# Kernel optimization log

Measured on AMD Instinct MI355X. Metric: run time of the kernel, lower is better.

Reference implementation:

```python
import jax, jax.numpy as jnp
import numpy as np

N_NODES = 20000
N_EDGES = 320000
D_IN = 128
D_OUT = 128
HEADS = 12
BN_EPS = 1e-5


def setup_inputs() -> dict:
    key = jax.random.key(0)
    ks = jax.random.split(key, 24)
    x = jax.random.normal(ks[0], (N_NODES, D_IN), dtype=jnp.float32)
    # edges guaranteed to have no self loops (so remove_self_loops is a no-op)
    src = jax.random.randint(ks[1], (N_EDGES,), 0, N_NODES, dtype=jnp.int32)
    off = jax.random.randint(ks[2], (N_EDGES,), 1, N_NODES, dtype=jnp.int32)
    dst = (src + off) % N_NODES
    edge_index = jnp.stack([src, dst], axis=0)
    inp = {"x": x, "edge_index": edge_index}
    # per-layer FeatureSteeredConvolution params (torch init: uniform weights, N(0,0.1) c/bias)
    dims_in = [D_IN, D_OUT, D_OUT]
    k = 3
    for li in range(3):
        din = dims_in[li]
        inp[f"l{li}_Wlin"] = jax.random.uniform(ks[k], (HEADS * D_OUT, din), dtype=jnp.float32); k += 1
        inp[f"l{li}_Wu"] = jax.random.uniform(ks[k], (HEADS, din), dtype=jnp.float32); k += 1
        inp[f"l{li}_c"] = 0.1 * jax.random.normal(ks[k], (HEADS,), dtype=jnp.float32); k += 1
        inp[f"l{li}_b"] = 0.1 * jax.random.normal(ks[k], (D_OUT,), dtype=jnp.float32); k += 1
    for bi in range(2):
        inp[f"bn{bi}_g"] = jnp.ones((D_OUT,), dtype=jnp.float32)
        inp[f"bn{bi}_b"] = jnp.zeros((D_OUT,), dtype=jnp.float32)
    return inp


def _fsc(x, src, dst, Wlin, Wu, c, b):
    """FeatureSteeredConvolution: edge gather -> softmax attention over heads ->
    per-head linear -> scatter-mean over destination nodes."""
    n = x.shape[0]
    x_j = x[src]                                  # [E, Cin] source features
    x_i = x[dst]                                  # [E, Cin] target features
    att = jax.nn.softmax((x_i - x_j) @ Wu.T + c, axis=1)   # [E, H]
    Wl = Wlin.reshape(HEADS, D_OUT, -1)           # [H, Cout, Cin]
    msg = jnp.zeros((src.shape[0], D_OUT), dtype=x.dtype)
    for h in range(HEADS):                        # small fixed loop over heads
        msg = msg + att[:, h:h + 1] * (x_j @ Wl[h].T)
    agg = jax.ops.segment_sum(msg, dst, num_segments=n)
    deg = jax.ops.segment_sum(jnp.ones((dst.shape[0],), dtype=x.dtype), dst, num_segments=n)
    return agg / jnp.maximum(deg, 1.0)[:, None] + b


def _bn(x, g, b):
    # BatchNorm1d in training mode: biased batch statistics
    m = jnp.mean(x, axis=0)
    v = jnp.var(x, axis=0)
    return (x - m) * jax.lax.rsqrt(v + BN_EPS) * g + b


def reference(x, edge_index, l0_Wlin, l0_Wu, l0_c, l0_b, bn0_g, bn0_b,
              l1_Wlin, l1_Wu, l1_c, l1_b, bn1_g, bn1_b,
              l2_Wlin, l2_Wu, l2_c, l2_b):
    n = x.shape[0]
    loops = jnp.arange(n, dtype=edge_index.dtype)
    src = jnp.concatenate([edge_index[0], loops])
    dst = jnp.concatenate([edge_index[1], loops])
    h = jax.nn.relu(_fsc(x, src, dst, l0_Wlin, l0_Wu, l0_c, l0_b))
    h = _bn(h, bn0_g, bn0_b)
    h = jax.nn.relu(_fsc(h, src, dst, l1_Wlin, l1_Wu, l1_c, l1_b))
    h = _bn(h, bn1_g, bn1_b)
    return _fsc(h, src, dst, l2_Wlin, l2_Wu, l2_c, l2_b)
```

## Files before the change

kernel.cpp:

```cpp
#include <hip/hip_runtime.h>
#include <hip/hip_bf16.h>

#define DHID 128
#define NH 12
#define KDIM 1536
#define KSPLIT 3
#define KS (KDIM / KSPLIT)
#define NSTATB 128

typedef __attribute__((ext_vector_type(8))) short short8;
typedef __attribute__((ext_vector_type(4))) float f32x4;

static __device__ __forceinline__ unsigned short f2bf(float f) {
  __hip_bfloat16 h = __float2bfloat16(f);
  return __builtin_bit_cast(unsigned short, h);
}


__global__ void hist_k(const int* __restrict__ dstp, int* __restrict__ cnt, int e0, int et) {
  int e = blockIdx.x * blockDim.x + threadIdx.x;
  if (e >= et) return;
  int d = (e < e0) ? dstp[e] : (e - e0);
  atomicAdd(&cnt[d], 1);
}

__global__ void scan_k(const int* __restrict__ cnt, int* __restrict__ row_start,
                       int* __restrict__ cursor, int n, int total) {
  __shared__ int part[1024];
  int t = threadIdx.x;
  const int CH = (n + 1023) >> 10;
  int base = t * CH;
  int s = 0;
  for (int j = 0; j < CH; ++j) { int i = base + j; if (i < n) s += cnt[i]; }
  part[t] = s;
  __syncthreads();
  for (int off = 1; off < 1024; off <<= 1) {
    int v = (t >= off) ? part[t - off] : 0;
    __syncthreads();
    part[t] += v;
    __syncthreads();
  }
  int run = (t == 0) ? 0 : part[t - 1];
  for (int j = 0; j < CH; ++j) {
    int i = base + j;
    if (i < n) {
      int c = cnt[i];
      row_start[i] = run;
      cursor[i] = run;
      run += c;
    }
  }
  if (t == 0) row_start[n] = total;
}

__global__ void scatter_k(const int* __restrict__ srcp, const int* __restrict__ dstp,
                          int* __restrict__ cursor, int* __restrict__ srcs,
                          int* __restrict__ dsts, int e0, int et) {
  int e = blockIdx.x * blockDim.x + threadIdx.x;
  if (e >= et) return;
  int s = (e < e0) ? srcp[e] : (e - e0);
  int d = (e < e0) ? dstp[e] : (e - e0);
  int pos = atomicAdd(&cursor[d], 1);
  srcs[pos] = s;
  dsts[pos] = d;
}


__global__ void u_k(const float* __restrict__ x, const float* __restrict__ Wu,
                    float* __restrict__ u, int n) {
  int wid = (blockIdx.x * blockDim.x + threadIdx.x) >> 6;
  if (wid >= n) return;
  int lane = threadIdx.x & 63;
  float2 xv = *(const float2*)(x + (long)wid * DHID + 2 * lane);
  #pragma unroll
  for (int h = 0; h < NH; ++h) {
    float2 wv = *(const float2*)(Wu + h * DHID + 2 * lane);
    float p = xv.x * wv.x + xv.y * wv.y;
    p += __shfl_xor(p, 1);  p += __shfl_xor(p, 2);  p += __shfl_xor(p, 4);
    p += __shfl_xor(p, 8);  p += __shfl_xor(p, 16); p += __shfl_xor(p, 32);
    if (lane == 0) u[wid * NH + h] = p;
  }
}


__global__ void att_k(const float* __restrict__ u, const float* __restrict__ cvec,
                      const int* __restrict__ srcs, const int* __restrict__ dsts,
                      const int* __restrict__ row_start, float* __restrict__ attS, int et) {
  int j = blockIdx.x * blockDim.x + threadIdx.x;
  if (j >= et) return;
  int s = srcs[j], d = dsts[j];
  const float4* ud = (const float4*)(u + (long)d * NH);
  const float4* us = (const float4*)(u + (long)s * NH);
  const float4* cp = (const float4*)cvec;
  float w[NH];
  #pragma unroll
  for (int q = 0; q < 3; ++q) {
    float4 a = ud[q], b = us[q], c = cp[q];
    w[4*q+0] = a.x - b.x + c.x;
    w[4*q+1] = a.y - b.y + c.y;
    w[4*q+2] = a.z - b.z + c.z;
    w[4*q+3] = a.w - b.w + c.w;
  }
  float m = w[0];
  #pragma unroll
  for (int h = 1; h < NH; ++h) m = fmaxf(m, w[h]);
  float ssum = 0.f;
  #pragma unroll
  for (int h = 0; h < NH; ++h) { w[h] = __expf(w[h] - m); ssum += w[h]; }
  float deg = (float)(row_start[d + 1] - row_start[d]);
  float inv = 1.f / (ssum * deg);
  float4* op = (float4*)(attS + (long)j * NH);
  #pragma unroll
  for (int q = 0; q < 3; ++q) {
    float4 v;
    v.x = w[4*q+0] * inv; v.y = w[4*q+1] * inv;
    v.z = w[4*q+2] * inv; v.w = w[4*q+3] * inv;
    op[q] = v;
  }
}


__global__ void edge_k(const float* __restrict__ x, const float* __restrict__ attS,
                       const int* __restrict__ srcs, const int* __restrict__ row_start,
                       unsigned short* __restrict__ A, int n) {
  int wid = __builtin_amdgcn_readfirstlane((int)((blockIdx.x * blockDim.x + threadIdx.x) >> 6));
  if (wid >= n) return;
  int lane = threadIdx.x & 63;
  float acc[NH][2];
  #pragma unroll
  for (int h = 0; h < NH; ++h) { acc[h][0] = 0.f; acc[h][1] = 0.f; }
  int beg = row_start[wid], end = row_start[wid + 1];
  int j = beg;
  for (; j + 3 < end; j += 4) {
    int sx[4];
    #pragma unroll
    for (int i = 0; i < 4; ++i) sx[i] = srcs[j + i];
    float2 xv[4];
    #pragma unroll
    for (int i = 0; i < 4; ++i)
      xv[i] = *(const float2*)(x + (long)sx[i] * DHID + 2 * lane);
    const float4* ap = (const float4*)(attS + (long)j * NH);
    float4 aq[4][3];
    #pragma unroll
    for (int i = 0; i < 4; ++i) {
      aq[i][0] = ap[i * 3 + 0];
      aq[i][1] = ap[i * 3 + 1];
      aq[i][2] = ap[i * 3 + 2];
    }
    #pragma unroll
    for (int i = 0; i < 4; ++i) {
      float av[NH];
      av[0]=aq[i][0].x; av[1]=aq[i][0].y; av[2] =aq[i][0].z; av[3] =aq[i][0].w;
      av[4]=aq[i][1].x; av[5]=aq[i][1].y; av[6] =aq[i][1].z; av[7] =aq[i][1].w;
      av[8]=aq[i][2].x; av[9]=aq[i][2].y; av[10]=aq[i][2].z; av[11]=aq[i][2].w;
      #pragma unroll
      for (int h = 0; h < NH; ++h) {
        acc[h][0] += av[h] * xv[i].x;
        acc[h][1] += av[h] * xv[i].y;
      }
    }
  }
  for (; j < end; ++j) {
    int s0 = srcs[j];
    float2 xv0 = *(const float2*)(x + (long)s0 * DHID + 2 * lane);
    const float4* a0p = (const float4*)(attS + (long)j * NH);
    float4 a00 = a0p[0], a01 = a0p[1], a02 = a0p[2];
    float av0[NH];
    av0[0]=a00.x; av0[1]=a00.y; av0[2]=a00.z;  av0[3]=a00.w;
    av0[4]=a01.x; av0[5]=a01.y; av0[6]=a01.z;  av0[7]=a01.w;
    av0[8]=a02.x; av0[9]=a02.y; av0[10]=a02.z; av0[11]=a02.w;
    #pragma unroll
    for (int h = 0; h < NH; ++h) {
      acc[h][0] += av0[h] * xv0.x;
      acc[h][1] += av0[h] * xv0.y;
    }
  }
  unsigned* Ap = (unsigned*)(A + (long)wid * KDIM);
  #pragma unroll
  for (int h = 0; h < NH; ++h) {
    unsigned pv = (unsigned)f2bf(acc[h][0]) | ((unsigned)f2bf(acc[h][1]) << 16);
    Ap[h * (DHID / 2) + lane] = pv;
  }
}


__global__ void prep_wcat_k(const float* __restrict__ Wlin, unsigned short* __restrict__ Wcat) {
  int t = blockIdx.x * blockDim.x + threadIdx.x;
  int c = t / KDIM, f = t - c * KDIM;
  int h = f >> 7, k = f & (DHID - 1);
  Wcat[t] = f2bf(Wlin[((h << 7) + c) * DHID + k]);
}


__global__ __launch_bounds__(256) void gemm_k(
    const unsigned short* __restrict__ A, const unsigned short* __restrict__ B,
    float* __restrict__ part, float* __restrict__ outp, int M) {
  int w = threadIdx.x >> 6, lane = threadIdx.x & 63;
  int lr = lane & 15, lq = lane >> 4;
  int m0 = blockIdx.x * 64, n0 = w * 32;
  int ks = blockIdx.y;
  if (m0 >= M) return;
  f32x4 acc[4][2];
  #pragma unroll
  for (int mf = 0; mf < 4; ++mf)
    #pragma unroll
    for (int nf = 0; nf < 2; ++nf) acc[mf][nf] = (f32x4){0.f, 0.f, 0.f, 0.f};
  const short* Ap = (const short*)A;
  const short* Bp = (const short*)B;
  long arow[4], brow[2];
  #pragma unroll
  for (int mf = 0; mf < 4; ++mf) arow[mf] = (long)(m0 + mf * 16 + lr) * KDIM + lq * 8;
  #pragma unroll
  for (int nf = 0; nf < 2; ++nf) brow[nf] = (long)(n0 + nf * 16 + lr) * KDIM + lq * 8;
  const int kbeg = ks * KS, kend = kbeg + KS;
  #pragma unroll 2
  for (int kk = kbeg; kk < kend; kk += 32) {
    short8 av[4], bv[2];
    #pragma unroll
    for (int mf = 0; mf < 4; ++mf) av[mf] = *(const short8*)(Ap + arow[mf] + kk);
    #pragma unroll
    for (int nf = 0; nf < 2; ++nf) bv[nf] = *(const short8*)(Bp + brow[nf] + kk);
    #pragma unroll
    for (int mf = 0; mf < 4; ++mf)
      #pragma unroll
      for (int nf = 0; nf < 2; ++nf)
        acc[mf][nf] = __builtin_amdgcn_mfma_f32_16x16x32_bf16(av[mf], bv[nf], acc[mf][nf], 0, 0, 0);
  }
  float* op = (ks == 0) ? outp : (part + (long)(ks - 1) * M * DHID);
  #pragma unroll
  for (int mf = 0; mf < 4; ++mf) {
    #pragma unroll
    for (int nf = 0; nf < 2; ++nf) {
      int c = n0 + nf * 16 + lr;
      int rowb = m0 + mf * 16 + lq * 4;
      #pragma unroll
      for (int r = 0; r < 4; ++r) {
        int row = rowb + r;
        if (row < M) op[(long)row * DHID + c] = acc[mf][nf][r];
      }
    }
  }
}


__global__ void combine_k(const float* __restrict__ part, const float* __restrict__ bias,
                          float* __restrict__ outp, int M, int relu) {
  int t = blockIdx.x * blockDim.x + threadIdx.x;
  int nvec = M * (DHID / 4);
  if (t >= nvec) return;
  long idx = (long)t * 4;
  int c = (t & 31) * 4;
  float4 p0 = *(const float4*)(outp + idx);
  float4 p1 = *(const float4*)(part + idx);
  float4 p2 = *(const float4*)(part + (long)M * DHID + idx);
  float4 bc = *(const float4*)(bias + c);
  float4 v;
  v.x = p0.x + p1.x + p2.x + bc.x;
  v.y = p0.y + p1.y + p2.y + bc.y;
  v.z = p0.z + p1.z + p2.z + bc.z;
  v.w = p0.w + p1.w + p2.w + bc.w;
  if (relu) {
    v.x = fmaxf(v.x, 0.f); v.y = fmaxf(v.y, 0.f);
    v.z = fmaxf(v.z, 0.f); v.w = fmaxf(v.w, 0.f);
  }
  *(float4*)(outp + idx) = v;
}


__global__ __launch_bounds__(256) void bnstat_k(const float* __restrict__ buf,
                                                float* __restrict__ bnpart, int nvec) {
  int t = blockIdx.x * 256 + threadIdx.x;
  const int stride = NSTATB * 256;
  float s0=0,s1=0,s2=0,s3=0,q0=0,q1=0,q2=0,q3=0;
  for (int i = t; i < nvec; i += stride) {
    float4 v = *(const float4*)(buf + (long)i * 4);
    s0 += v.x; s1 += v.y; s2 += v.z; s3 += v.w;
    q0 += v.x*v.x; q1 += v.y*v.y; q2 += v.z*v.z; q3 += v.w*v.w;
  }
  s0 += __shfl_xor(s0, 32); s1 += __shfl_xor(s1, 32);
  s2 += __shfl_xor(s2, 32); s3 += __shfl_xor(s3, 32);
  q0 += __shfl_xor(q0, 32); q1 += __shfl_xor(q1, 32);
  q2 += __shfl_xor(q2, 32); q3 += __shfl_xor(q3, 32);
  __shared__ float red[4][256];
  int w = threadIdx.x >> 6, lane = threadIdx.x & 63;
  if (lane < 32) {
    int cb = lane * 4;
    red[w][cb+0] = s0; red[w][cb+1] = s1; red[w][cb+2] = s2; red[w][cb+3] = s3;
    red[w][128+cb+0] = q0; red[w][128+cb+1] = q1; red[w][128+cb+2] = q2; red[w][128+cb+3] = q3;
  }
  __syncthreads();
  int tt = threadIdx.x;
  float p = red[0][tt] + red[1][tt] + red[2][tt] + red[3][tt];
  bnpart[blockIdx.x * 256 + tt] = p;
}


__global__ void bnfin_k(const float* __restrict__ bnpart,
                        const float* __restrict__ g, const float* __restrict__ b,
                        float* __restrict__ sc, float* __restrict__ sh, float invn) {
  __shared__ float col[256];
  int t = threadIdx.x;
  float s = 0.f;
  #pragma unroll 8
  for (int bb = 0; bb < NSTATB; ++bb) s += bnpart[bb * 256 + t];
  col[t] = s;
  __syncthreads();
  if (t < DHID) {
    float m = col[t] * invn;
    float v = col[128 + t] * invn - m * m;
    float rs = rsqrtf(v + 1e-5f);
    float sg = g[t] * rs;
    sc[t] = sg;
    sh[t] = b[t] - m * sg;
  }
}

__global__ void bnapply_k(float* __restrict__ buf, const float* __restrict__ sc,
                          const float* __restrict__ sh, int nvec) {
  int i = blockIdx.x * blockDim.x + threadIdx.x;
  if (i >= nvec) return;
  long idx = (long)i * 4;
  int c = (int)(idx & (DHID - 1));
  float4 v = *(const float4*)(buf + idx);
  v.x = v.x * sc[c]     + sh[c];
  v.y = v.y * sc[c + 1] + sh[c + 1];
  v.z = v.z * sc[c + 2] + sh[c + 2];
  v.w = v.w * sc[c + 3] + sh[c + 3];
  *(float4*)(buf + idx) = v;
}


extern "C" void kernel_launch(void* const* d_in, const int* in_sizes, int n_in,
                              void* d_out, int out_size, void* d_ws, size_t ws_size,
                              hipStream_t stream) {
  const float* x = (const float*)d_in[0];
  const int* ei = (const int*)d_in[1];
  const int N = in_sizes[0] / DHID;
  const int E0 = in_sizes[1] / 2;
  const int ET = E0 + N;
  const int* srcp = ei;
  const int* dstp = ei + E0;
  const float* Wlin[3] = {(const float*)d_in[2], (const float*)d_in[6], (const float*)d_in[10]};
  const float* Wu[3]   = {(const float*)d_in[3], (const float*)d_in[7], (const float*)d_in[11]};
  const float* cc[3]   = {(const float*)d_in[4], (const float*)d_in[8], (const float*)d_in[12]};
  const float* bb[3]   = {(const float*)d_in[5], (const float*)d_in[9], (const float*)d_in[13]};
  const float* bng[2]  = {(const float*)d_in[14], (const float*)d_in[16]};
  const float* bnb[2]  = {(const float*)d_in[15], (const float*)d_in[17]};

  const int MPAD = ((N + 63) / 64) * 64;

  size_t o = 0;
  char* base = (char*)d_ws;
  auto carve = [&](size_t bytes) -> char* {
    char* p = base + o;
    o += (bytes + 255) & ~(size_t)255;
    return p;
  };
  int* row_start = (int*)carve((size_t)(N + 1) * 4);
  int* cursor    = (int*)carve((size_t)N * 4);
  int* srcs      = (int*)carve((size_t)ET * 4);
  int* dsts      = (int*)carve((size_t)ET * 4);
  float* u       = (float*)carve((size_t)N * NH * 4);
  float* bnpart  = (float*)carve((size_t)NSTATB * 256 * 4);
  float* bnsc    = (float*)carve((size_t)DHID * 4);
  float* bnsh    = (float*)carve((size_t)DHID * 4);
  unsigned short* Wcat = (unsigned short*)carve((size_t)DHID * KDIM * 2);
  size_t attS_bytes = (size_t)ET * NH * 4;
  size_t part_bytes = (size_t)(KSPLIT - 1) * N * DHID * 4;
  char* shared_rg = carve(attS_bytes > part_bytes ? attS_bytes : part_bytes);
  float* attS = (float*)shared_rg;
  float* partb = (float*)shared_rg;
  float* hA      = (float*)carve((size_t)N * DHID * 4);
  unsigned short* A = (unsigned short*)carve((size_t)MPAD * KDIM * 2);
  (void)ws_size; (void)n_in; (void)out_size;

  const int EB = (ET + 255) / 256;
  const int NW = (N + 3) / 4;
  const int MB64 = (N + 63) / 64;
  const int AV = (N * DHID / 4 + 255) / 256;

  hipMemsetAsync(cursor, 0, (size_t)N * 4, stream);
  hist_k<<<EB, 256, 0, stream>>>(dstp, cursor, E0, ET);
  scan_k<<<1, 1024, 0, stream>>>(cursor, row_start, cursor, N, ET);
  scatter_k<<<EB, 256, 0, stream>>>(srcp, dstp, cursor, srcs, dsts, E0, ET);

  const float* hin = x;
  for (int li = 0; li < 3; ++li) {
    const bool last = (li == 2);
    u_k<<<NW, 256, 0, stream>>>(hin, Wu[li], u, N);
    att_k<<<EB, 256, 0, stream>>>(u, cc[li], srcs, dsts, row_start, attS, ET);
    edge_k<<<NW, 256, 0, stream>>>(hin, attS, srcs, row_start, A, N);
    prep_wcat_k<<<(DHID * KDIM) / 256, 256, 0, stream>>>(Wlin[li], Wcat);
    float* outp = last ? (float*)d_out : hA;
    gemm_k<<<dim3(MB64, KSPLIT), 256, 0, stream>>>(A, Wcat, partb, outp, N);
    combine_k<<<AV, 256, 0, stream>>>(partb, bb[li], outp, N, last ? 0 : 1);
    if (!last) {
      bnstat_k<<<NSTATB, 256, 0, stream>>>(hA, bnpart, N * DHID / 4);
      bnfin_k<<<1, 256, 0, stream>>>(bnpart, bng[li], bnb[li], bnsc, bnsh, 1.f / (float)N);
      bnapply_k<<<AV, 256, 0, stream>>>(hA, bnsc, bnsh, N * DHID / 4);
      hin = hA;
    }
  }
}
```

Baseline: 543.1 us.

## Fuse BN stats into combine, fold BN apply into bf16 feature cast, prefetch GEMM

Batch-norm statistics are now accumulated inside the split-K combine kernel, and the BN scale/shift is applied inside u_k. u_k also writes a bf16 copy of the node features, so the separate bnstat and bnapply passes over the hidden buffer are removed. edge_k gathers the bf16 features instead of fp32, halving the gather bytes per edge. The GEMM inner loop now software-prefetches the next K slice into registers. The gathered features lose precision to bf16 before aggregation, and the combine runs as a fixed-size grid-stride kernel.

```diff
diff --git a/kernel.cpp b/kernel.cpp
--- a/kernel.cpp
+++ b/kernel.cpp
@@ -5,8 +5,8 @@
 #define NH 12
 #define KDIM 1536
 #define KSPLIT 3
-#define KS (KDIM / KSPLIT)
-#define NSTATB 128
+#define KSL (KDIM / KSPLIT)
+#define COMBB 512
 
 typedef __attribute__((ext_vector_type(8))) short short8;
 typedef __attribute__((ext_vector_type(4))) float f32x4;
@@ -14,6 +14,10 @@
 static __device__ __forceinline__ unsigned short f2bf(float f) {
   __hip_bfloat16 h = __float2bfloat16(f);
   return __builtin_bit_cast(unsigned short, h);
+}
+static __device__ __forceinline__ float bf2f(unsigned short u) {
+  unsigned v = ((unsigned)u) << 16;
+  return __builtin_bit_cast(float, v);
 }
 
 
@@ -66,12 +70,22 @@
 }
 
 
-__global__ void u_k(const float* __restrict__ x, const float* __restrict__ Wu,
-                    float* __restrict__ u, int n) {
+template<int BN>
+__global__ void u_k(const float* __restrict__ in, const float* __restrict__ Wu,
+                    const float* __restrict__ sc, const float* __restrict__ sh,
+                    unsigned short* __restrict__ xb, float* __restrict__ u, int n) {
   int wid = (blockIdx.x * blockDim.x + threadIdx.x) >> 6;
   if (wid >= n) return;
   int lane = threadIdx.x & 63;
-  float2 xv = *(const float2*)(x + (long)wid * DHID + 2 * lane);
+  float2 xv = *(const float2*)(in + (long)wid * DHID + 2 * lane);
+  if (BN) {
+    float2 scv = *(const float2*)(sc + 2 * lane);
+    float2 shv = *(const float2*)(sh + 2 * lane);
+    xv.x = xv.x * scv.x + shv.x;
+    xv.y = xv.y * scv.y + shv.y;
+  }
+  unsigned pv = (unsigned)f2bf(xv.x) | ((unsigned)f2bf(xv.y) << 16);
+  *(unsigned*)(xb + (long)wid * DHID + 2 * lane) = pv;
   #pragma unroll
   for (int h = 0; h < NH; ++h) {
     float2 wv = *(const float2*)(Wu + h * DHID + 2 * lane);
@@ -120,7 +134,7 @@
 }
 
 
-__global__ void edge_k(const float* __restrict__ x, const float* __restrict__ attS,
+__global__ void edge_k(const unsigned short* __restrict__ xb, const float* __restrict__ attS,
                        const int* __restrict__ srcs, const int* __restrict__ row_start,
                        unsigned short* __restrict__ A, int n) {
   int wid = __builtin_amdgcn_readfirstlane((int)((blockIdx.x * blockDim.x + threadIdx.x) >> 6));
@@ -135,10 +149,10 @@
     int sx[4];
     #pragma unroll
     for (int i = 0; i < 4; ++i) sx[i] = srcs[j + i];
-    float2 xv[4];
+    unsigned pv[4];
     #pragma unroll
     for (int i = 0; i < 4; ++i)
-      xv[i] = *(const float2*)(x + (long)sx[i] * DHID + 2 * lane);
+      pv[i] = *(const unsigned*)(xb + (long)sx[i] * DHID + 2 * lane);
     const float4* ap = (const float4*)(attS + (long)j * NH);
     float4 aq[4][3];
     #pragma unroll
@@ -149,20 +163,24 @@
     }
     #pragma unroll
     for (int i = 0; i < 4; ++i) {
+      float xv0 = bf2f((unsigned short)pv[i]);
+      float xv1 = bf2f((unsigned short)(pv[i] >> 16));
       float av[NH];
       av[0]=aq[i][0].x; av[1]=aq[i][0].y; av[2] =aq[i][0].z; av[3] =aq[i][0].w;
       av[4]=aq[i][1].x; av[5]=aq[i][1].y; av[6] =aq[i][1].z; av[7] =aq[i][1].w;
       av[8]=aq[i][2].x; av[9]=aq[i][2].y; av[10]=aq[i][2].z; av[11]=aq[i][2].w;
       #pragma unroll
       for (int h = 0; h < NH; ++h) {
-        acc[h][0] += av[h] * xv[i].x;
-        acc[h][1] += av[h] * xv[i].y;
+        acc[h][0] += av[h] * xv0;
+        acc[h][1] += av[h] * xv1;
       }
     }
   }
   for (; j < end; ++j) {
     int s0 = srcs[j];
-    float2 xv0 = *(const float2*)(x + (long)s0 * DHID + 2 * lane);
+    unsigned pv = *(const unsigned*)(xb + (long)s0 * DHID + 2 * lane);
+    float xv0 = bf2f((unsigned short)pv);
+    float xv1 = bf2f((unsigned short)(pv >> 16));
     const float4* a0p = (const float4*)(attS + (long)j * NH);
     float4 a00 = a0p[0], a01 = a0p[1], a02 = a0p[2];
     float av0[NH];
@@ -171,8 +189,8 @@
     av0[8]=a02.x; av0[9]=a02.y; av0[10]=a02.z; av0[11]=a02.w;
     #pragma unroll
     for (int h = 0; h < NH; ++h) {
-      acc[h][0] += av0[h] * xv0.x;
-      acc[h][1] += av0[h] * xv0.y;
+      acc[h][0] += av0[h] * xv0;
+      acc[h][1] += av0[h] * xv1;
     }
   }
   unsigned* Ap = (unsigned*)(A + (long)wid * KDIM);
@@ -207,24 +225,34 @@
     for (int nf = 0; nf < 2; ++nf) acc[mf][nf] = (f32x4){0.f, 0.f, 0.f, 0.f};
   const short* Ap = (const short*)A;
   const short* Bp = (const short*)B;
+  const long kbeg = (long)ks * KSL;
   long arow[4], brow[2];
   #pragma unroll
-  for (int mf = 0; mf < 4; ++mf) arow[mf] = (long)(m0 + mf * 16 + lr) * KDIM + lq * 8;
-  #pragma unroll
-  for (int nf = 0; nf < 2; ++nf) brow[nf] = (long)(n0 + nf * 16 + lr) * KDIM + lq * 8;
-  const int kbeg = ks * KS, kend = kbeg + KS;
+  for (int mf = 0; mf < 4; ++mf) arow[mf] = (long)(m0 + mf * 16 + lr) * KDIM + lq * 8 + kbeg;
+  #pragma unroll
+  for (int nf = 0; nf < 2; ++nf) brow[nf] = (long)(n0 + nf * 16 + lr) * KDIM + lq * 8 + kbeg;
+  short8 ac[4], bc[2];
+  #pragma unroll
+  for (int mf = 0; mf < 4; ++mf) ac[mf] = *(const short8*)(Ap + arow[mf]);
+  #pragma unroll
+  for (int nf = 0; nf < 2; ++nf) bc[nf] = *(const short8*)(Bp + brow[nf]);
   #pragma unroll 2
-  for (int kk = kbeg; kk < kend; kk += 32) {
-    short8 av[4], bv[2];
-    #pragma unroll
-    for (int mf = 0; mf < 4; ++mf) av[mf] = *(const short8*)(Ap + arow[mf] + kk);
-    #pragma unroll
-    for (int nf = 0; nf < 2; ++nf) bv[nf] = *(const short8*)(Bp + brow[nf] + kk);
+  for (int kk = 0; kk < KSL; kk += 32) {
+    const int kn = (kk + 32 < KSL) ? (kk + 32) : kk;
+    short8 an[4], bn[2];
+    #pragma unroll
+    for (int mf = 0; mf < 4; ++mf) an[mf] = *(const short8*)(Ap + arow[mf] + kn);
+    #pragma unroll
+    for (int nf = 0; nf < 2; ++nf) bn[nf] = *(const short8*)(Bp + brow[nf] + kn);
     #pragma unroll
     for (int mf = 0; mf < 4; ++mf)
       #pragma unroll
       for (int nf = 0; nf < 2; ++nf)
-        acc[mf][nf] = __builtin_amdgcn_mfma_f32_16x16x32_bf16(av[mf], bv[nf], acc[mf][nf], 0, 0, 0);
+        acc[mf][nf] = __builtin_amdgcn_mfma_f32_16x16x32_bf16(ac[mf], bc[nf], acc[mf][nf], 0, 0, 0);
+    #pragma unroll
+    for (int mf = 0; mf < 4; ++mf) ac[mf] = an[mf];
+    #pragma unroll
+    for (int nf = 0; nf < 2; ++nf) bc[nf] = bn[nf];
   }
   float* op = (ks == 0) ? outp : (part + (long)(ks - 1) * M * DHID);
   #pragma unroll
@@ -243,55 +271,51 @@
 }
 
 
-__global__ void combine_k(const float* __restrict__ part, const float* __restrict__ bias,
-                          float* __restrict__ outp, int M, int relu) {
-  int t = blockIdx.x * blockDim.x + threadIdx.x;
-  int nvec = M * (DHID / 4);
-  if (t >= nvec) return;
-  long idx = (long)t * 4;
-  int c = (t & 31) * 4;
-  float4 p0 = *(const float4*)(outp + idx);
-  float4 p1 = *(const float4*)(part + idx);
-  float4 p2 = *(const float4*)(part + (long)M * DHID + idx);
+template<int RELU, int DOBN>
+__global__ __launch_bounds__(256) void combine_k(
+    const float* __restrict__ part, const float* __restrict__ bias,
+    float* __restrict__ outp, float* __restrict__ bnpart, int M) {
+  const int nvec = M * (DHID / 4);
+  const int stride = COMBB * 256;
+  int t0 = blockIdx.x * 256 + threadIdx.x;
+  int c = (t0 & 31) * 4;
   float4 bc = *(const float4*)(bias + c);
-  float4 v;
-  v.x = p0.x + p1.x + p2.x + bc.x;
-  v.y = p0.y + p1.y + p2.y + bc.y;
-  v.z = p0.z + p1.z + p2.z + bc.z;
-  v.w = p0.w + p1.w + p2.w + bc.w;
-  if (relu) {
-    v.x = fmaxf(v.x, 0.f); v.y = fmaxf(v.y, 0.f);
-    v.z = fmaxf(v.z, 0.f); v.w = fmaxf(v.w, 0.f);
-  }
-  *(float4*)(outp + idx) = v;
-}
-
-
-__global__ __launch_bounds__(256) void bnstat_k(const float* __restrict__ buf,
-                                                float* __restrict__ bnpart, int nvec) {
-  int t = blockIdx.x * 256 + threadIdx.x;
-  const int stride = NSTATB * 256;
   float s0=0,s1=0,s2=0,s3=0,q0=0,q1=0,q2=0,q3=0;
-  for (int i = t; i < nvec; i += stride) {
-    float4 v = *(const float4*)(buf + (long)i * 4);
-    s0 += v.x; s1 += v.y; s2 += v.z; s3 += v.w;
-    q0 += v.x*v.x; q1 += v.y*v.y; q2 += v.z*v.z; q3 += v.w*v.w;
-  }
-  s0 += __shfl_xor(s0, 32); s1 += __shfl_xor(s1, 32);
-  s2 += __shfl_xor(s2, 32); s3 += __shfl_xor(s3, 32);
-  q0 += __shfl_xor(q0, 32); q1 += __shfl_xor(q1, 32);
-  q2 += __shfl_xor(q2, 32); q3 += __shfl_xor(q3, 32);
-  __shared__ float red[4][256];
-  int w = threadIdx.x >> 6, lane = threadIdx.x & 63;
-  if (lane < 32) {
-    int cb = lane * 4;
-    red[w][cb+0] = s0; red[w][cb+1] = s1; red[w][cb+2] = s2; red[w][cb+3] = s3;
-    red[w][128+cb+0] = q0; red[w][128+cb+1] = q1; red[w][128+cb+2] = q2; red[w][128+cb+3] = q3;
-  }
-  __syncthreads();
-  int tt = threadIdx.x;
-  float p = red[0][tt] + red[1][tt] + red[2][tt] + red[3][tt];
-  bnpart[blockIdx.x * 256 + tt] = p;
+  for (int t = t0; t < nvec; t += stride) {
+    long idx = (long)t * 4;
+    float4 v  = *(const float4*)(outp + idx);
+    float4 p1 = *(const float4*)(part + idx);
+    float4 p2 = *(const float4*)(part + (long)M * DHID + idx);
+    v.x += p1.x + p2.x + bc.x;
+    v.y += p1.y + p2.y + bc.y;
+    v.z += p1.z + p2.z + bc.z;
+    v.w += p1.w + p2.w + bc.w;
+    if (RELU) {
+      v.x = fmaxf(v.x, 0.f); v.y = fmaxf(v.y, 0.f);
+      v.z = fmaxf(v.z, 0.f); v.w = fmaxf(v.w, 0.f);
+    }
+    *(float4*)(outp + idx) = v;
+    if (DOBN) {
+      s0 += v.x; s1 += v.y; s2 += v.z; s3 += v.w;
+      q0 += v.x*v.x; q1 += v.y*v.y; q2 += v.z*v.z; q3 += v.w*v.w;
+    }
+  }
+  if (DOBN) {
+    s0 += __shfl_xor(s0, 32); s1 += __shfl_xor(s1, 32);
+    s2 += __shfl_xor(s2, 32); s3 += __shfl_xor(s3, 32);
+    q0 += __shfl_xor(q0, 32); q1 += __shfl_xor(q1, 32);
+    q2 += __shfl_xor(q2, 32); q3 += __shfl_xor(q3, 32);
+    __shared__ float red[4][256];
+    int w = threadIdx.x >> 6, lane = threadIdx.x & 63;
+    if (lane < 32) {
+      int cb = lane * 4;
+      red[w][cb+0] = s0; red[w][cb+1] = s1; red[w][cb+2] = s2; red[w][cb+3] = s3;
+      red[w][128+cb+0] = q0; red[w][128+cb+1] = q1; red[w][128+cb+2] = q2; red[w][128+cb+3] = q3;
+    }
+    __syncthreads();
+    int tt = threadIdx.x;
+    bnpart[blockIdx.x * 256 + tt] = red[0][tt] + red[1][tt] + red[2][tt] + red[3][tt];
+  }
 }
 
 
@@ -302,7 +326,7 @@
   int t = threadIdx.x;
   float s = 0.f;
   #pragma unroll 8
-  for (int bb = 0; bb < NSTATB; ++bb) s += bnpart[bb * 256 + t];
+  for (int bb = 0; bb < COMBB; ++bb) s += bnpart[bb * 256 + t];
   col[t] = s;
   __syncthreads();
   if (t < DHID) {
@@ -313,20 +337,6 @@
     sc[t] = sg;
     sh[t] = b[t] - m * sg;
   }
-}
-
-__global__ void bnapply_k(float* __restrict__ buf, const float* __restrict__ sc,
-                          const float* __restrict__ sh, int nvec) {
-  int i = blockIdx.x * blockDim.x + threadIdx.x;
-  if (i >= nvec) return;
-  long idx = (long)i * 4;
-  int c = (int)(idx & (DHID - 1));
-  float4 v = *(const float4*)(buf + idx);
-  v.x = v.x * sc[c]     + sh[c];
-  v.y = v.y * sc[c + 1] + sh[c + 1];
-  v.z = v.z * sc[c + 2] + sh[c + 2];
-  v.w = v.w * sc[c + 3] + sh[c + 3];
-  *(float4*)(buf + idx) = v;
 }
 
 
@@ -361,44 +371,43 @@
   int* srcs      = (int*)carve((size_t)ET * 4);
   int* dsts      = (int*)carve((size_t)ET * 4);
   float* u       = (float*)carve((size_t)N * NH * 4);
-  float* bnpart  = (float*)carve((size_t)NSTATB * 256 * 4);
+  float* bnpart  = (float*)carve((size_t)COMBB * 256 * 4);
   float* bnsc    = (float*)carve((size_t)DHID * 4);
   float* bnsh    = (float*)carve((size_t)DHID * 4);
   unsigned short* Wcat = (unsigned short*)carve((size_t)DHID * KDIM * 2);
+  float* hA      = (float*)carve((size_t)N * DHID * 4);
+  unsigned short* xb = (unsigned short*)carve((size_t)N * DHID * 2);
+  unsigned short* A  = (unsigned short*)carve((size_t)MPAD * KDIM * 2);
   size_t attS_bytes = (size_t)ET * NH * 4;
   size_t part_bytes = (size_t)(KSPLIT - 1) * N * DHID * 4;
   char* shared_rg = carve(attS_bytes > part_bytes ? attS_bytes : part_bytes);
   float* attS = (float*)shared_rg;
   float* partb = (float*)shared_rg;
-  float* hA      = (float*)carve((size_t)N * DHID * 4);
-  unsigned short* A = (unsigned short*)carve((size_t)MPAD * KDIM * 2);
   (void)ws_size; (void)n_in; (void)out_size;
 
   const int EB = (ET + 255) / 256;
   const int NW = (N + 3) / 4;
   const int MB64 = (N + 63) / 64;
-  const int AV = (N * DHID / 4 + 255) / 256;
 
   hipMemsetAsync(cursor, 0, (size_t)N * 4, stream);
   hist_k<<<EB, 256, 0, stream>>>(dstp, cursor, E0, ET);
   scan_k<<<1, 1024, 0, stream>>>(cursor, row_start, cursor, N, ET);
   scatter_k<<<EB, 256, 0, stream>>>(srcp, dstp, cursor, srcs, dsts, E0, ET);
 
-  const float* hin = x;
   for (int li = 0; li < 3; ++li) {
     const bool last = (li == 2);
-    u_k<<<NW, 256, 0, stream>>>(hin, Wu[li], u, N);
+    if (li == 0) u_k<0><<<NW, 256, 0, stream>>>(x, Wu[0], bnsc, bnsh, xb, u, N);
+    else         u_k<1><<<NW, 256, 0, stream>>>(hA, Wu[li], bnsc, bnsh, xb, u, N);
     att_k<<<EB, 256, 0, stream>>>(u, cc[li], srcs, dsts, row_start, attS, ET);
-    edge_k<<<NW, 256, 0, stream>>>(hin, attS, srcs, row_start, A, N);
+    edge_k<<<NW, 256, 0, stream>>>(xb, attS, srcs, row_start, A, N);
     prep_wcat_k<<<(DHID * KDIM) / 256, 256, 0, stream>>>(Wlin[li], Wcat);
     float* outp = last ? (float*)d_out : hA;
     gemm_k<<<dim3(MB64, KSPLIT), 256, 0, stream>>>(A, Wcat, partb, outp, N);
-    combine_k<<<AV, 256, 0, stream>>>(partb, bb[li], outp, N, last ? 0 : 1);
     if (!last) {
-      bnstat_k<<<NSTATB, 256, 0, stream>>>(hA, bnpart, N * DHID / 4);
+      combine_k<1, 1><<<COMBB, 256, 0, stream>>>(partb, bb[li], outp, bnpart, N);
       bnfin_k<<<1, 256, 0, stream>>>(bnpart, bng[li], bnb[li], bnsc, bnsh, 1.f / (float)N);
-      bnapply_k<<<AV, 256, 0, stream>>>(hA, bnsc, bnsh, N * DHID / 4);
-      hin = hA;
-    }
-  }
-}
+    } else {
+      combine_k<0, 0><<<COMBB, 256, 0, stream>>>(partb, bb[li], outp, bnpart, N);
+    }
+  }
+}
```

New measurement: 542.1 us. No clear change (-0.2%).
